# Kernel tuning notes

Measured on AMD Instinct MI355X. Metric: run time of the kernel, lower is better.

The kernel has to match this reference:

```python
import jax, jax.numpy as jnp
import numpy as np

N = 100000   # nodes
E = 1600000  # edges
F_IN = 128
H = 128
C_OUT = 10
G = 128      # graphs in batch
EPS = 1e-5


def setup_inputs() -> dict:
    key = jax.random.key(0)
    ks = jax.random.split(key, 16)
    x = jax.random.normal(ks[0], (N, F_IN), dtype=jnp.float32)
    edge_index = jax.random.randint(ks[1], (2, E), 0, N, dtype=jnp.int64)
    batch = jnp.sort(jax.random.randint(ks[2], (N,), 0, G, dtype=jnp.int64))
    s = 1.0 / np.sqrt(H)
    inp = {"x": x, "edge_index": edge_index, "batch": batch}
    # GCNConv weights/biases
    inp["w1"] = jax.random.normal(ks[3], (F_IN, H), jnp.float32) * s
    inp["b1"] = jax.random.normal(ks[4], (H,), jnp.float32) * 0.01
    inp["w2"] = jax.random.normal(ks[5], (H, H), jnp.float32) * s
    inp["b2"] = jax.random.normal(ks[6], (H,), jnp.float32) * 0.01
    inp["w3"] = jax.random.normal(ks[7], (H, H), jnp.float32) * s
    inp["b3"] = jax.random.normal(ks[8], (H,), jnp.float32) * 0.01
    # GraphNorm params: scale (weight), shift (bias), mean_scale (alpha)
    for i, k in zip((1, 2, 3), (ks[9], ks[10], ks[11])):
        kk = jax.random.split(k, 3)
        inp[f"g{i}w"] = 1.0 + 0.1 * jax.random.normal(kk[0], (H,), jnp.float32)
        inp[f"g{i}b"] = 0.1 * jax.random.normal(kk[1], (H,), jnp.float32)
        inp[f"g{i}a"] = 1.0 + 0.1 * jax.random.normal(kk[2], (H,), jnp.float32)
    inp["lw"] = jax.random.normal(ks[12], (H, C_OUT), jnp.float32) * s
    inp["lb"] = jax.random.normal(ks[13], (C_OUT,), jnp.float32) * 0.01
    return inp


def _gcn_norm(edge_index, n):
    # add self loops, symmetric normalization D^-1/2 (A+I) D^-1/2
    loop = jnp.arange(n, dtype=edge_index.dtype)
    src = jnp.concatenate([edge_index[0], loop])
    dst = jnp.concatenate([edge_index[1], loop])
    deg = jax.ops.segment_sum(jnp.ones_like(dst, dtype=jnp.float32), dst, num_segments=n)
    dinv = jnp.where(deg > 0, jax.lax.rsqrt(deg), 0.0)
    norm = dinv[src] * dinv[dst]
    return src, dst, norm


def _gcn_conv(x, w, b, src, dst, norm, n):
    h = x @ w                              # [N,H]
    msg = h[src] * norm[:, None]           # gather + edge weight
    out = jax.ops.segment_sum(msg, dst, num_segments=n)  # scatter-add
    return out + b


def _graph_norm(x, weight, bias, alpha, batch, cnt, g):
    mean = jax.ops.segment_sum(x, batch, num_segments=g) / cnt[:, None]
    sub = x - alpha * mean[batch]
    var = jax.ops.segment_sum(sub * sub, batch, num_segments=g) / cnt[:, None]
    return weight * sub * jax.lax.rsqrt(var[batch] + EPS) + bias


def reference(x, edge_index, batch, w1, b1, w2, b2, w3, b3,
              g1w, g1b, g1a, g2w, g2b, g2a, g3w, g3b, g3a, lw, lb):
    n = x.shape[0]
    src, dst, norm = _gcn_norm(edge_index, n)
    cnt = jnp.maximum(jax.ops.segment_sum(jnp.ones((n,), jnp.float32), batch, num_segments=G), 1.0)
    # dropout is identity in eval mode
    h = _gcn_conv(x, w1, b1, src, dst, norm, n)
    h = jax.nn.relu(_graph_norm(h, g1w, g1b, g1a, batch, cnt, G))
    h = _gcn_conv(h, w2, b2, src, dst, norm, n)
    h = jax.nn.relu(_graph_norm(h, g2w, g2b, g2a, batch, cnt, G))
    h = _gcn_conv(h, w3, b3, src, dst, norm, n)
    h = jax.nn.relu(_graph_norm(h, g3w, g3b, g3a, batch, cnt, G))
    pooled = jax.ops.segment_sum(h, batch, num_segments=G) / cnt[:, None]  # global_mean_pool
    logits = pooled @ lw + lb
    return jax.nn.log_softmax(logits, axis=1)
```

## Files before the change

### kernel.cpp

```cpp
#include <hip/hip_runtime.h>

#define NN 100000
#define NE 1600000
#define HD 128
#define NG 128
#define NC 10
#define EPSV 1e-5f

#define BSH 9
#define NBKT ((NN + 511) >> 9)
#define BIN_BLOCKS ((NE + 4095) / 4096)

typedef __attribute__((ext_vector_type(8))) short short8;
typedef __attribute__((ext_vector_type(4))) float f32x4;

__device__ __forceinline__ float b2f(ushort u){ return __uint_as_float(((unsigned)u)<<16); }
__device__ __forceinline__ ushort f2b(float f){
  unsigned u = __float_as_uint(f);
  unsigned r = (u + 0x7FFFu + ((u>>16)&1u)) >> 16;
  return (ushort)r;
}

__global__ __launch_bounds__(256)
void k_init(const int* __restrict__ batch, int* __restrict__ gstart,
            const float* __restrict__ w1, const float* __restrict__ w2,
            const float* __restrict__ w3, ushort* __restrict__ wT,
            int* __restrict__ gbhist, float* __restrict__ zero_base)
{
  int b = blockIdx.x, t = threadIdx.x;
  if(b < 391){
    int n = b*256 + t;
    if(n >= NN) return;
    int bb = batch[n];
    if(n == 0){
      for(int g=0; g<=bb; g++) gstart[g] = 0;
      int last = batch[NN-1];
      for(int g=last+1; g<=NG; g++) gstart[g] = NN;
    } else {
      int bp = batch[n-1];
      for(int g=bp+1; g<=bb; g++) gstart[g] = n;
    }
  } else if(b < 394){
    const float* w = (b == 391) ? w1 : (b == 392) ? w2 : w3;
    ushort* o = wT + (b-391)*16384;
    #pragma unroll 4
    for(int i=0;i<64;i++){
      int e = i*256 + t;
      int k = e>>7, h = e&127;
      o[h*128 + k] = f2b(w[e]);
    }
  } else if(b < 408){
    #pragma unroll 8
    for(int i=0;i<32;i++) zero_base[(size_t)(b-394)*8192 + i*256 + t] = 0.f;
  } else {
    if(t < NBKT) gbhist[t] = 0;
  }
}

__global__ __launch_bounds__(256) void k_bhist(const int* __restrict__ ei, int* __restrict__ gbhist){
  __shared__ int h[NBKT];
  int t = threadIdx.x;
  if(t < NBKT) h[t] = 0;
  __syncthreads();
  int base = blockIdx.x*4096;
  #pragma unroll
  for(int i=0;i<16;i++){
    int e = base + i*256 + t;
    if(e < NE) atomicAdd(&h[ei[NE + e] >> BSH], 1);
  }
  __syncthreads();
  if(t < NBKT && h[t]) atomicAdd(&gbhist[t], h[t]);
}

__global__ void k_bscan(const int* __restrict__ gbhist, int* __restrict__ bucket_base,
                        int* __restrict__ bucket_cursor, int* __restrict__ rowstart){
  __shared__ int lds[256];
  int t = threadIdx.x;
  int v = (t < NBKT) ? gbhist[t] : 0;
  lds[t] = v; __syncthreads();
  for(int off=1; off<256; off<<=1){
    int y = lds[t]; int z = (t>=off)?lds[t-off]:0;
    __syncthreads(); lds[t] = y+z; __syncthreads();
  }
  int excl = (t>0)?lds[t-1]:0;
  if(t < NBKT){ bucket_base[t] = excl; bucket_cursor[t] = excl; }
  if(t == 0){ bucket_base[NBKT] = NE; rowstart[NN] = NE; }
}

__global__ __launch_bounds__(256) void k_bin(const int* __restrict__ ei, int* __restrict__ bucket_cursor,
                                             unsigned* __restrict__ ebuf){
  __shared__ unsigned eb[4096];
  __shared__ unsigned char bb4[4096];
  __shared__ int hist[NBKT], lstart[NBKT], lcur[NBKT], rbase[NBKT];
  __shared__ int scanbuf[256];
  int t = threadIdx.x;
  if(t < NBKT) hist[t] = 0;
  __syncthreads();
  int base = blockIdx.x*4096;
  int nv = NE - base; if(nv > 4096) nv = 4096;
  int se[16], de[16];
  #pragma unroll
  for(int i=0;i<16;i++){
    int e = base + i*256 + t;
    if(e < NE){ se[i] = ei[e]; de[i] = ei[NE + e]; atomicAdd(&hist[de[i] >> BSH], 1); }
  }
  __syncthreads();
  int v = (t < NBKT) ? hist[t] : 0;
  scanbuf[t] = v; __syncthreads();
  for(int off=1; off<256; off<<=1){
    int y = scanbuf[t]; int z = (t>=off)?scanbuf[t-off]:0;
    __syncthreads(); scanbuf[t] = y+z; __syncthreads();
  }
  if(t < NBKT){
    int excl = (t>0)?scanbuf[t-1]:0;
    lstart[t] = excl; lcur[t] = excl;
    if(hist[t]) rbase[t] = atomicAdd(&bucket_cursor[t], hist[t]);
  }
  __syncthreads();
  #pragma unroll
  for(int i=0;i<16;i++){
    int e = base + i*256 + t;
    if(e < NE){
      int b = de[i] >> BSH;
      int idx = atomicAdd(&lcur[b], 1);
      eb[idx] = ((unsigned)(de[i] & 511) << 17) | (unsigned)se[i];
      bb4[idx] = (unsigned char)b;
    }
  }
  __syncthreads();
  #pragma unroll
  for(int i=0;i<16;i++){
    int slot = i*256 + t;
    if(slot < nv){
      int b = bb4[slot];
      ebuf[rbase[b] + (slot - lstart[b])] = eb[slot];
    }
  }
}

__global__ __launch_bounds__(256) void k_sort(const unsigned* __restrict__ ebuf,
                                              const int* __restrict__ bucket_base,
                                              int* __restrict__ srcs, int* __restrict__ rowstart,
                                              float* __restrict__ dinv){
  __shared__ int hist[512], cur[512];
  __shared__ int scanbuf[256];
  int b = blockIdx.x, t = threadIdx.x;
  int e0 = bucket_base[b], e1 = bucket_base[b+1];
  hist[t] = 0; hist[t+256] = 0;
  __syncthreads();
  for(int i = e0 + t; i < e1; i += 256){
    atomicAdd(&hist[ebuf[i] >> 17], 1);
  }
  __syncthreads();
  int s0 = hist[2*t], s1 = hist[2*t+1];
  scanbuf[t] = s0 + s1; __syncthreads();
  for(int off=1; off<256; off<<=1){
    int y = scanbuf[t]; int z = (t>=off)?scanbuf[t-off]:0;
    __syncthreads(); scanbuf[t] = y+z; __syncthreads();
  }
  int excl = (t>0)?scanbuf[t-1]:0;
  cur[2*t] = excl; cur[2*t+1] = excl + s0;
  int d0 = (b << BSH) + 2*t, d1 = d0 + 1;
  if(d0 < NN){ rowstart[d0] = e0 + excl;      dinv[d0] = rsqrtf((float)(s0 + 1)); }
  if(d1 < NN){ rowstart[d1] = e0 + excl + s0; dinv[d1] = rsqrtf((float)(s1 + 1)); }
  __syncthreads();
  for(int i = e0 + t; i < e1; i += 256){
    unsigned pk = ebuf[i];
    int dl = pk >> 17;
    int pos = e0 + atomicAdd(&cur[dl], 1);
    srcs[pos] = (int)(pk & 0x1FFFFu);
  }
}

template<int NORM>
__global__ __launch_bounds__(256)
void k_gemm(const void* __restrict__ in_, const ushort* __restrict__ wT,
            ushort* __restrict__ g, const float* __restrict__ dinv,
            const int* __restrict__ batch,
            const float* __restrict__ gw, const float* __restrict__ gb,
            const float* __restrict__ ga, const float* __restrict__ S1,
            const float* __restrict__ S2, const int* __restrict__ gstart)
{
  __shared__ ushort lds_a[128*136];
  __shared__ float sdinv[128];
  const int t = threadIdx.x;
  const int row0 = blockIdx.x * 128;

  {
    const int l = t & 31;
    const int rr = t >> 5;
    if(t < 128){
      int node = row0 + t;
      sdinv[t] = (node < NN) ? dinv[node] : 0.f;
    }
    float4 gwv, gbv, gav;
    float4 amv = make_float4(0.f,0.f,0.f,0.f), rsv = make_float4(0.f,0.f,0.f,0.f);
    int gprev = -1;
    if(NORM){
      gwv = ((const float4*)gw)[l]; gbv = ((const float4*)gb)[l];
      gav = ((const float4*)ga)[l];
    }
    #pragma unroll 4
    for(int rb = 0; rb < 16; rb++){
      int r = rb*8 + rr;
      int node = row0 + r;
      float4 v = make_float4(0.f,0.f,0.f,0.f);
      if(node < NN){
        if(NORM){
          ushort4 raw = ((const ushort4*)in_)[(size_t)node*32 + l];
          v = make_float4(b2f(raw.x), b2f(raw.y), b2f(raw.z), b2f(raw.w));
          int gg = batch[node];
          if(gg != gprev){
            gprev = gg;
            int c0 = gstart[gg], c1 = gstart[gg+1];
            float inv = 1.f/(float)((c1-c0) > 0 ? (c1-c0) : 1);
            float4 s1v = ((const float4*)S1)[gg*32 + l];
            float4 s2v = ((const float4*)S2)[gg*32 + l];
            float m, ex2, a;
            m = s1v.x*inv; ex2 = s2v.x*inv; a = gav.x;
            amv.x = a*m; rsv.x = rsqrtf(ex2 - (2.f*a - a*a)*m*m + EPSV);
            m = s1v.y*inv; ex2 = s2v.y*inv; a = gav.y;
            amv.y = a*m; rsv.y = rsqrtf(ex2 - (2.f*a - a*a)*m*m + EPSV);
            m = s1v.z*inv; ex2 = s2v.z*inv; a = gav.z;
            amv.z = a*m; rsv.z = rsqrtf(ex2 - (2.f*a - a*a)*m*m + EPSV);
            m = s1v.w*inv; ex2 = s2v.w*inv; a = gav.w;
            amv.w = a*m; rsv.w = rsqrtf(ex2 - (2.f*a - a*a)*m*m + EPSV);
          }
          v.x = fmaxf(gwv.x*(v.x-amv.x)*rsv.x + gbv.x, 0.f);
          v.y = fmaxf(gwv.y*(v.y-amv.y)*rsv.y + gbv.y, 0.f);
          v.z = fmaxf(gwv.z*(v.z-amv.z)*rsv.z + gbv.z, 0.f);
          v.w = fmaxf(gwv.w*(v.w-amv.w)*rsv.w + gbv.w, 0.f);
        } else {
          v = ((const float4*)in_)[(size_t)node*32 + l];
        }
      }
      ushort4 b4;
      b4.x = f2b(v.x); b4.y = f2b(v.y); b4.z = f2b(v.z); b4.w = f2b(v.w);
      *(ushort4*)(lds_a + r*136 + l*4) = b4;
    }
  }
  __syncthreads();

  const int wv = t >> 6;
  const int l  = t & 63;
  const int lc = l & 15, lk = l >> 4;

  short8 bfrag[2][4];
  #pragma unroll
  for(int tt=0; tt<2; tt++){
    int col = wv*32 + tt*16 + lc;
    #pragma unroll
    for(int s=0; s<4; s++)
      bfrag[tt][s] = *(const short8*)(wT + col*128 + s*32 + lk*8);
  }

  f32x4 acc[8][2];
  #pragma unroll
  for(int m=0;m<8;m++){ acc[m][0] = (f32x4)0.f; acc[m][1] = (f32x4)0.f; }

  #pragma unroll
  for(int m=0; m<8; m++){
    const ushort* ap = lds_a + (m*16 + lc)*136 + lk*8;
    #pragma unroll
    for(int s=0; s<4; s++){
      short8 a = *(const short8*)(ap + s*32);
      acc[m][0] = __builtin_amdgcn_mfma_f32_16x16x32_bf16(a, bfrag[0][s], acc[m][0], 0, 0, 0);
      acc[m][1] = __builtin_amdgcn_mfma_f32_16x16x32_bf16(a, bfrag[1][s], acc[m][1], 0, 0, 0);
    }
  }

  #pragma unroll
  for(int m=0; m<8; m++){
    #pragma unroll
    for(int tt=0; tt<2; tt++){
      int colg = wv*32 + tt*16 + lc;
      #pragma unroll
      for(int r=0; r<4; r++){
        int row = m*16 + lk*4 + r;
        int node = row0 + row;
        if(node < NN)
          g[(size_t)node*128 + colg] = f2b(acc[m][tt][r] * sdinv[row]);
      }
    }
  }
}

__global__ __launch_bounds__(256)
void k_agg(const ushort* __restrict__ g, const int* __restrict__ rowstart,
           const int* __restrict__ srcs, const float* __restrict__ dinv,
           const float* __restrict__ bias, ushort* __restrict__ outp)
{
  const int lane = threadIdx.x & 31;
  const int node = blockIdx.x*8 + (threadIdx.x >> 5);
  const int e0 = rowstart[node], e1 = rowstart[node+1];
  float ax=0.f, ay=0.f, az=0.f, aw=0.f;
  float bx=0.f, by=0.f, bz=0.f, bw=0.f;
  const ushort4* gp = (const ushort4*)g;
  int e = e0;
  for(; e+7 < e1; e += 8){
    int si[8];
    #pragma unroll
    for(int i=0;i<8;i++) si[i] = srcs[e+i];
    ushort4 v[8];
    #pragma unroll
    for(int i=0;i<8;i++) v[i] = gp[(size_t)si[i]*32 + lane];
    #pragma unroll
    for(int i=0;i<8;i++){
      if(i&1){ bx += b2f(v[i].x); by += b2f(v[i].y); bz += b2f(v[i].z); bw += b2f(v[i].w); }
      else   { ax += b2f(v[i].x); ay += b2f(v[i].y); az += b2f(v[i].z); aw += b2f(v[i].w); }
    }
  }
  for(; e+3 < e1; e += 4){
    int si[4];
    #pragma unroll
    for(int i=0;i<4;i++) si[i] = srcs[e+i];
    ushort4 v[4];
    #pragma unroll
    for(int i=0;i<4;i++) v[i] = gp[(size_t)si[i]*32 + lane];
    #pragma unroll
    for(int i=0;i<4;i++){
      if(i&1){ bx += b2f(v[i].x); by += b2f(v[i].y); bz += b2f(v[i].z); bw += b2f(v[i].w); }
      else   { ax += b2f(v[i].x); ay += b2f(v[i].y); az += b2f(v[i].z); aw += b2f(v[i].w); }
    }
  }
  for(; e < e1; e++){
    ushort4 v = gp[(size_t)srcs[e]*32 + lane];
    ax += b2f(v.x); ay += b2f(v.y); az += b2f(v.z); aw += b2f(v.w);
  }
  ushort4 vs = gp[(size_t)node*32 + lane];
  float dv = dinv[node];
  float4 bv = ((const float4*)bias)[lane];
  ushort4 o4;
  o4.x = f2b(dv*(ax+bx+b2f(vs.x))+bv.x);
  o4.y = f2b(dv*(ay+by+b2f(vs.y))+bv.y);
  o4.z = f2b(dv*(az+bz+b2f(vs.z))+bv.z);
  o4.w = f2b(dv*(aw+bw+b2f(vs.w))+bv.w);
  ((ushort4*)outp)[(size_t)node*32 + lane] = o4;
}

#define STAT_CH 8
__global__ __launch_bounds__(128)
void k_stats(const ushort* __restrict__ x, const int* __restrict__ gstart,
             float* __restrict__ S1, float* __restrict__ S2)
{
  int g = blockIdx.x, ch = blockIdx.y, f = threadIdx.x;
  int s = gstart[g], e = gstart[g+1];
  int len = e - s;
  int i0 = s + (int)((long long)len * ch / STAT_CH);
  int i1 = s + (int)((long long)len * (ch+1) / STAT_CH);
  float a1 = 0.f, a2 = 0.f;
  for(int n=i0; n<i1; n++){
    float v = b2f(x[(size_t)n*128 + f]);
    a1 += v; a2 += v*v;
  }
  if(i1 > i0){
    atomicAdd(&S1[g*128+f], a1);
    atomicAdd(&S2[g*128+f], a2);
  }
}

#define POOL_CH 16
__global__ __launch_bounds__(128)
void k_pool(const ushort* __restrict__ x, const int* __restrict__ gstart,
            const float* __restrict__ gw, const float* __restrict__ gb,
            const float* __restrict__ ga, const float* __restrict__ S1,
            const float* __restrict__ S2, float* __restrict__ pooled)
{
  int g = blockIdx.x, ch = blockIdx.y, f = threadIdx.x;
  int s = gstart[g], e = gstart[g+1];
  int len = e - s;
  int i0 = s + (int)((long long)len * ch / POOL_CH);
  int i1 = s + (int)((long long)len * (ch+1) / POOL_CH);
  float inv = 1.f/(float)(len > 0 ? len : 1);
  float a = ga[f];
  float m = S1[g*128+f]*inv, ex2 = S2[g*128+f]*inv;
  float am = a*m;
  float rs = rsqrtf(ex2 - (2.f*a - a*a)*m*m + EPSV);
  float wv = gw[f], bv = gb[f];
  float a1 = 0.f;
  for(int n=i0; n<i1; n++){
    float v = b2f(x[(size_t)n*128 + f]);
    v = wv*(v-am)*rs + bv;
    a1 += fmaxf(v, 0.f);
  }
  if(i1 > i0) atomicAdd(&pooled[g*128+f], a1);
}

__global__ __launch_bounds__(64)
void k_head(const float* __restrict__ pooled, const int* __restrict__ gstart,
            const float* __restrict__ lw, const float* __restrict__ lb,
            float* __restrict__ out)
{
  int g = blockIdx.x, t = threadIdx.x;
  __shared__ float lg[NC];
  __shared__ float lse_s;
  int len = gstart[g+1] - gstart[g];
  float inv = 1.f/(float)(len > 0 ? len : 1);
  if(t < NC){
    float acc = lb[t];
    for(int f=0; f<128; f++) acc += pooled[g*128+f]*inv*lw[f*NC + t];
    lg[t] = acc;
  }
  __syncthreads();
  if(t == 0){
    float mx = -1e30f;
    for(int c=0;c<NC;c++) mx = fmaxf(mx, lg[c]);
    float sm = 0.f;
    for(int c=0;c<NC;c++) sm += expf(lg[c]-mx);
    lse_s = mx + logf(sm);
  }
  __syncthreads();
  if(t < NC) out[g*NC + t] = lg[t] - lse_s;
}

extern "C" void kernel_launch(void* const* d_in, const int* in_sizes, int n_in,
                              void* d_out, int out_size, void* d_ws, size_t ws_size,
                              hipStream_t stream)
{
  const float* x    = (const float*)d_in[0];
  const int*   ei   = (const int*)d_in[1];
  const int*   batch= (const int*)d_in[2];
  const float* w1   = (const float*)d_in[3];
  const float* b1   = (const float*)d_in[4];
  const float* w2   = (const float*)d_in[5];
  const float* b2   = (const float*)d_in[6];
  const float* w3   = (const float*)d_in[7];
  const float* b3   = (const float*)d_in[8];
  const float* g1w  = (const float*)d_in[9];
  const float* g1b  = (const float*)d_in[10];
  const float* g1a  = (const float*)d_in[11];
  const float* g2w  = (const float*)d_in[12];
  const float* g2b  = (const float*)d_in[13];
  const float* g2a  = (const float*)d_in[14];
  const float* g3w  = (const float*)d_in[15];
  const float* g3b  = (const float*)d_in[16];
  const float* g3a  = (const float*)d_in[17];
  const float* lw   = (const float*)d_in[18];
  const float* lb   = (const float*)d_in[19];
  float* out = (float*)d_out;

  char* p = (char*)d_ws;
  auto take = [&](size_t nbytes){ char* q = p; p += (nbytes + 255) & ~(size_t)255; return q; };
  ushort* gbuf    = (ushort*)take((size_t)NN*HD*2);
  ushort* bufB    = (ushort*)take((size_t)NN*HD*2);
  ushort* wT      = (ushort*)take((size_t)3*HD*HD*2);
  unsigned* ebuf  = (unsigned*)take((size_t)NE*4);
  int*   srcs     = (int*)  take((size_t)NE*4);
  int*   rowstart = (int*)  take((size_t)(NN+1)*4);
  float* dinv     = (float*)take((size_t)NN*4);
  int*   gbhist   = (int*)  take((size_t)NBKT*4);
  int*   bucket_base   = (int*)take((size_t)(NBKT+1)*4);
  int*   bucket_cursor = (int*)take((size_t)NBKT*4);
  int*   gstart   = (int*)  take((size_t)(NG+1)*4);
  float* Sbase    = (float*)take((size_t)(3*2*NG*HD + NG*HD)*4);
  if((size_t)(p - (char*)d_ws) > ws_size) return;

  float* SL1 = Sbase;
  float* SL2 = Sbase + 2*NG*HD;
  float* SL3 = Sbase + 4*NG*HD;
  float* pooled = Sbase + 6*NG*HD;

  k_init  <<<409, 256, 0, stream>>>(batch, gstart, w1, w2, w3, wT, gbhist, Sbase);
  k_bhist <<<BIN_BLOCKS, 256, 0, stream>>>(ei, gbhist);
  k_bscan <<<1, 256, 0, stream>>>(gbhist, bucket_base, bucket_cursor, rowstart);
  k_bin   <<<BIN_BLOCKS, 256, 0, stream>>>(ei, bucket_cursor, ebuf);
  k_sort  <<<NBKT, 256, 0, stream>>>(ebuf, bucket_base, srcs, rowstart, dinv);

  const int GB = (NN + 127)/128;
  const int AB = NN/8;

  k_gemm<0><<<GB, 256, 0, stream>>>(x, wT, gbuf, dinv, batch,
                                    nullptr, nullptr, nullptr, nullptr, nullptr, gstart);
  k_agg<<<AB, 256, 0, stream>>>(gbuf, rowstart, srcs, dinv, b1, bufB);
  k_stats<<<dim3(NG, STAT_CH), 128, 0, stream>>>(bufB, gstart, SL1, SL1 + NG*HD);

  k_gemm<1><<<GB, 256, 0, stream>>>(bufB, wT + 16384, gbuf, dinv, batch,
                                    g1w, g1b, g1a, SL1, SL1 + NG*HD, gstart);
  k_agg<<<AB, 256, 0, stream>>>(gbuf, rowstart, srcs, dinv, b2, bufB);
  k_stats<<<dim3(NG, STAT_CH), 128, 0, stream>>>(bufB, gstart, SL2, SL2 + NG*HD);

  k_gemm<1><<<GB, 256, 0, stream>>>(bufB, wT + 32768, gbuf, dinv, batch,
                                    g2w, g2b, g2a, SL2, SL2 + NG*HD, gstart);
  k_agg<<<AB, 256, 0, stream>>>(gbuf, rowstart, srcs, dinv, b3, bufB);
  k_stats<<<dim3(NG, STAT_CH), 128, 0, stream>>>(bufB, gstart, SL3, SL3 + NG*HD);

  k_pool<<<dim3(NG, POOL_CH), 128, 0, stream>>>(bufB, gstart, g3w, g3b, g3a,
                                                SL3, SL3 + NG*HD, pooled);
  k_head<<<NG, 64, 0, stream>>>(pooled, gstart, lw, lb, out);
}
```

Measured before the change: 436.5 us.

## Fuse preprocessing and per-layer stages into persistent cooperative kernels with grid syncs

Replaces the five preprocessing launches with one cooperative kernel that uses grid.sync between init, histogram, scan, bin and sort phases. It also merges each layer's gemm, aggregation and stats launches, plus pool and head on the last layer, into one persistent cooperative kernel that loops over tiles. The gemm tile shrinks to 64 rows, and B fragments are loaded once per block. The aim is to remove per-kernel launch gaps and tail effects, at the cost of grid-wide barrier overhead and lower parallelism in the small phases. If a cooperative launch fails, the code falls back to the original separate kernels.

```diff
diff --git a/kernel.cpp b/kernel.cpp
--- a/kernel.cpp
+++ b/kernel.cpp
@@ -1,4 +1,7 @@
 #include <hip/hip_runtime.h>
+#include <hip/hip_cooperative_groups.h>
+
+namespace cg = cooperative_groups;
 
 #define NN 100000
 #define NE 1600000
@@ -10,6 +13,8 @@
 #define BSH 9
 #define NBKT ((NN + 511) >> 9)
 #define BIN_BLOCKS ((NE + 4095) / 4096)
+#define STAT_CH 8
+#define POOL_CH 16
 
 typedef __attribute__((ext_vector_type(8))) short short8;
 typedef __attribute__((ext_vector_type(4))) float f32x4;
@@ -20,6 +25,40 @@
   unsigned r = (u + 0x7FFFu + ((u>>16)&1u)) >> 16;
   return (ushort)r;
 }
+
+
+__device__ __forceinline__ void init_body(int vb, int t, const int* batch, int* gstart,
+    const float* w1, const float* w2, const float* w3, ushort* wT, int* gbhist, float* zero_base)
+{
+  if(vb < 391){
+    int n = vb*256 + t;
+    if(n < NN){
+      int bb = batch[n];
+      if(n == 0){
+        for(int g=0; g<=bb; g++) gstart[g] = 0;
+        int last = batch[NN-1];
+        for(int g=last+1; g<=NG; g++) gstart[g] = NN;
+      } else {
+        int bp = batch[n-1];
+        for(int g=bp+1; g<=bb; g++) gstart[g] = n;
+      }
+    }
+  } else if(vb < 394){
+    const float* w = (vb == 391) ? w1 : (vb == 392) ? w2 : w3;
+    ushort* o = wT + (vb-391)*16384;
+    #pragma unroll 4
+    for(int i=0;i<64;i++){
+      int e = i*256 + t;
+      o[(e & 127)*128 + (e >> 7)] = f2b(w[e]);
+    }
+  } else if(vb < 408){
+    #pragma unroll 8
+    for(int i=0;i<32;i++) zero_base[(size_t)(vb-394)*8192 + i*256 + t] = 0.f;
+  } else {
+    if(t < NBKT) gbhist[t] = 0;
+  }
+}
+
 
 __global__ __launch_bounds__(256)
 void k_init(const int* __restrict__ batch, int* __restrict__ gstart,
@@ -27,34 +66,7 @@
             const float* __restrict__ w3, ushort* __restrict__ wT,
             int* __restrict__ gbhist, float* __restrict__ zero_base)
 {
-  int b = blockIdx.x, t = threadIdx.x;
-  if(b < 391){
-    int n = b*256 + t;
-    if(n >= NN) return;
-    int bb = batch[n];
-    if(n == 0){
-      for(int g=0; g<=bb; g++) gstart[g] = 0;
-      int last = batch[NN-1];
-      for(int g=last+1; g<=NG; g++) gstart[g] = NN;
-    } else {
-      int bp = batch[n-1];
-      for(int g=bp+1; g<=bb; g++) gstart[g] = n;
-    }
-  } else if(b < 394){
-    const float* w = (b == 391) ? w1 : (b == 392) ? w2 : w3;
-    ushort* o = wT + (b-391)*16384;
-    #pragma unroll 4
-    for(int i=0;i<64;i++){
-      int e = i*256 + t;
-      int k = e>>7, h = e&127;
-      o[h*128 + k] = f2b(w[e]);
-    }
-  } else if(b < 408){
-    #pragma unroll 8
-    for(int i=0;i<32;i++) zero_base[(size_t)(b-394)*8192 + i*256 + t] = 0.f;
-  } else {
-    if(t < NBKT) gbhist[t] = 0;
-  }
+  init_body(blockIdx.x, threadIdx.x, batch, gstart, w1, w2, w3, wT, gbhist, zero_base);
 }
 
 __global__ __launch_bounds__(256) void k_bhist(const int* __restrict__ ei, int* __restrict__ gbhist){
@@ -148,9 +160,8 @@
   int e0 = bucket_base[b], e1 = bucket_base[b+1];
   hist[t] = 0; hist[t+256] = 0;
   __syncthreads();
-  for(int i = e0 + t; i < e1; i += 256){
+  for(int i = e0 + t; i < e1; i += 256)
     atomicAdd(&hist[ebuf[i] >> 17], 1);
-  }
   __syncthreads();
   int s0 = hist[2*t], s1 = hist[2*t+1];
   scanbuf[t] = s0 + s1; __syncthreads();
@@ -185,7 +196,6 @@
   __shared__ float sdinv[128];
   const int t = threadIdx.x;
   const int row0 = blockIdx.x * 128;
-
   {
     const int l = t & 31;
     const int rr = t >> 5;
@@ -241,10 +251,7 @@
   }
   __syncthreads();
 
-  const int wv = t >> 6;
-  const int l  = t & 63;
-  const int lc = l & 15, lk = l >> 4;
-
+  const int wv = t >> 6, l = t & 63, lc = l & 15, lk = l >> 4;
   short8 bfrag[2][4];
   #pragma unroll
   for(int tt=0; tt<2; tt++){
@@ -253,11 +260,9 @@
     for(int s=0; s<4; s++)
       bfrag[tt][s] = *(const short8*)(wT + col*128 + s*32 + lk*8);
   }
-
   f32x4 acc[8][2];
   #pragma unroll
   for(int m=0;m<8;m++){ acc[m][0] = (f32x4)0.f; acc[m][1] = (f32x4)0.f; }
-
   #pragma unroll
   for(int m=0; m<8; m++){
     const ushort* ap = lds_a + (m*16 + lc)*136 + lk*8;
@@ -268,7 +273,6 @@
       acc[m][1] = __builtin_amdgcn_mfma_f32_16x16x32_bf16(a, bfrag[1][s], acc[m][1], 0, 0, 0);
     }
   }
-
   #pragma unroll
   for(int m=0; m<8; m++){
     #pragma unroll
@@ -338,7 +342,6 @@
   ((ushort4*)outp)[(size_t)node*32 + lane] = o4;
 }
 
-#define STAT_CH 8
 __global__ __launch_bounds__(128)
 void k_stats(const ushort* __restrict__ x, const int* __restrict__ gstart,
              float* __restrict__ S1, float* __restrict__ S2)
@@ -359,7 +362,6 @@
   }
 }
 
-#define POOL_CH 16
 __global__ __launch_bounds__(128)
 void k_pool(const ushort* __restrict__ x, const int* __restrict__ gstart,
             const float* __restrict__ gw, const float* __restrict__ gb,
@@ -411,6 +413,372 @@
   }
   __syncthreads();
   if(t < NC) out[g*NC + t] = lg[t] - lse_s;
+}
+
+
+__global__ __launch_bounds__(256)
+void k_prep(const int* __restrict__ ei, const int* __restrict__ batch, int* __restrict__ gstart,
+            const float* __restrict__ w1, const float* __restrict__ w2, const float* __restrict__ w3,
+            ushort* __restrict__ wT, int* __restrict__ gbhist, float* __restrict__ zero_base,
+            int* __restrict__ bucket_base, int* __restrict__ bucket_cursor, int* __restrict__ rowstart,
+            unsigned* __restrict__ ebuf, int* __restrict__ srcs, float* __restrict__ dinv)
+{
+  __shared__ unsigned eb[4096];
+  __shared__ unsigned char bb4[4096];
+  __shared__ int hist[512];
+  __shared__ int cur[512];
+  __shared__ int lstart[NBKT];
+  __shared__ int rbase[NBKT];
+  __shared__ int scanbuf[256];
+  cg::grid_group grid = cg::this_grid();
+  const int t = threadIdx.x;
+
+  for(int vb = blockIdx.x; vb < 409; vb += gridDim.x)
+    init_body(vb, t, batch, gstart, w1, w2, w3, wT, gbhist, zero_base);
+  grid.sync();
+
+  for(int vb = blockIdx.x; vb < BIN_BLOCKS; vb += gridDim.x){
+    if(t < NBKT) hist[t] = 0;
+    __syncthreads();
+    int base = vb*4096;
+    #pragma unroll
+    for(int i=0;i<16;i++){
+      int e = base + i*256 + t;
+      if(e < NE) atomicAdd(&hist[ei[NE + e] >> BSH], 1);
+    }
+    __syncthreads();
+    if(t < NBKT && hist[t]) atomicAdd(&gbhist[t], hist[t]);
+    __syncthreads();
+  }
+  grid.sync();
+
+  if(blockIdx.x == 0){
+    int v = (t < NBKT) ? gbhist[t] : 0;
+    scanbuf[t] = v; __syncthreads();
+    for(int off=1; off<256; off<<=1){
+      int y = scanbuf[t]; int z = (t>=off)?scanbuf[t-off]:0;
+      __syncthreads(); scanbuf[t] = y+z; __syncthreads();
+    }
+    int excl = (t>0)?scanbuf[t-1]:0;
+    if(t < NBKT){ bucket_base[t] = excl; bucket_cursor[t] = excl; }
+    if(t == 0){ bucket_base[NBKT] = NE; rowstart[NN] = NE; }
+  }
+  grid.sync();
+
+  for(int vb = blockIdx.x; vb < BIN_BLOCKS; vb += gridDim.x){
+    if(t < NBKT) hist[t] = 0;
+    __syncthreads();
+    int base = vb*4096;
+    int nv = NE - base; if(nv > 4096) nv = 4096;
+    int se[16], de[16];
+    #pragma unroll
+    for(int i=0;i<16;i++){
+      int e = base + i*256 + t;
+      if(e < NE){ se[i] = ei[e]; de[i] = ei[NE + e]; atomicAdd(&hist[de[i] >> BSH], 1); }
+    }
+    __syncthreads();
+    int v = (t < NBKT) ? hist[t] : 0;
+    scanbuf[t] = v; __syncthreads();
+    for(int off=1; off<256; off<<=1){
+      int y = scanbuf[t]; int z = (t>=off)?scanbuf[t-off]:0;
+      __syncthreads(); scanbuf[t] = y+z; __syncthreads();
+    }
+    if(t < NBKT){
+      int excl = (t>0)?scanbuf[t-1]:0;
+      lstart[t] = excl; cur[t] = excl;
+      if(hist[t]) rbase[t] = atomicAdd(&bucket_cursor[t], hist[t]);
+    }
+    __syncthreads();
+    #pragma unroll
+    for(int i=0;i<16;i++){
+      int e = base + i*256 + t;
+      if(e < NE){
+        int b = de[i] >> BSH;
+        int idx = atomicAdd(&cur[b], 1);
+        eb[idx] = ((unsigned)(de[i] & 511) << 17) | (unsigned)se[i];
+        bb4[idx] = (unsigned char)b;
+      }
+    }
+    __syncthreads();
+    #pragma unroll
+    for(int i=0;i<16;i++){
+      int slot = i*256 + t;
+      if(slot < nv){
+        int b = bb4[slot];
+        ebuf[rbase[b] + (slot - lstart[b])] = eb[slot];
+      }
+    }
+    __syncthreads();
+  }
+  grid.sync();
+
+  for(int vb = blockIdx.x; vb < NBKT; vb += gridDim.x){
+    int e0 = bucket_base[vb], e1 = bucket_base[vb+1];
+    hist[t] = 0; hist[t+256] = 0;
+    __syncthreads();
+    for(int i = e0 + t; i < e1; i += 256)
+      atomicAdd(&hist[ebuf[i] >> 17], 1);
+    __syncthreads();
+    int s0 = hist[2*t], s1 = hist[2*t+1];
+    scanbuf[t] = s0 + s1; __syncthreads();
+    for(int off=1; off<256; off<<=1){
+      int y = scanbuf[t]; int z = (t>=off)?scanbuf[t-off]:0;
+      __syncthreads(); scanbuf[t] = y+z; __syncthreads();
+    }
+    int excl = (t>0)?scanbuf[t-1]:0;
+    cur[2*t] = excl; cur[2*t+1] = excl + s0;
+    int d0 = (vb << BSH) + 2*t, d1 = d0 + 1;
+    if(d0 < NN){ rowstart[d0] = e0 + excl;      dinv[d0] = rsqrtf((float)(s0 + 1)); }
+    if(d1 < NN){ rowstart[d1] = e0 + excl + s0; dinv[d1] = rsqrtf((float)(s1 + 1)); }
+    __syncthreads();
+    for(int i = e0 + t; i < e1; i += 256){
+      unsigned pk = ebuf[i];
+      int dl = pk >> 17;
+      int pos = e0 + atomicAdd(&cur[dl], 1);
+      srcs[pos] = (int)(pk & 0x1FFFFu);
+    }
+    __syncthreads();
+  }
+}
+
+template<int NORM, int LAST>
+__global__ __launch_bounds__(256, 4)
+void k_layer(const void* in_, const ushort* __restrict__ wTl,
+             ushort* gbuf, ushort* outB,
+             const float* __restrict__ dinv, const int* __restrict__ batch,
+             const int* __restrict__ gstart, const int* __restrict__ rowstart,
+             const int* __restrict__ srcs, const float* __restrict__ bias,
+             const float* __restrict__ gw, const float* __restrict__ gb,
+             const float* __restrict__ ga, const float* S1p, const float* S2p,
+             float* S1c, float* S2c,
+             const float* __restrict__ pw, const float* __restrict__ pb,
+             const float* __restrict__ pa, float* __restrict__ pooled,
+             const float* __restrict__ lw, const float* __restrict__ lb,
+             float* __restrict__ out)
+{
+  __shared__ ushort lds_a[64*136];
+  __shared__ float sdinv[64];
+  __shared__ float shead[NC+1];
+  cg::grid_group grid = cg::this_grid();
+  const int t = threadIdx.x;
+  const int wv = t >> 6, l = t & 63, lc = l & 15, lk = l >> 4;
+
+  short8 bfrag[2][4];
+  #pragma unroll
+  for(int tt=0; tt<2; tt++){
+    int col = wv*32 + tt*16 + lc;
+    #pragma unroll
+    for(int s=0; s<4; s++)
+      bfrag[tt][s] = *(const short8*)(wTl + col*128 + s*32 + lk*8);
+  }
+
+  for(int tile = blockIdx.x; tile < (NN+63)/64; tile += gridDim.x){
+    const int row0 = tile * 64;
+    {
+      const int sl = t & 31;
+      const int rr = t >> 5;
+      if(t < 64){
+        int node = row0 + t;
+        sdinv[t] = (node < NN) ? dinv[node] : 0.f;
+      }
+      float4 gwv, gbv, gav;
+      float4 amv = make_float4(0.f,0.f,0.f,0.f), rsv = make_float4(0.f,0.f,0.f,0.f);
+      int gprev = -1;
+      if(NORM){
+        gwv = ((const float4*)gw)[sl]; gbv = ((const float4*)gb)[sl];
+        gav = ((const float4*)ga)[sl];
+      }
+      #pragma unroll 4
+      for(int rb = 0; rb < 8; rb++){
+        int r = rb*8 + rr;
+        int node = row0 + r;
+        float4 v = make_float4(0.f,0.f,0.f,0.f);
+        if(node < NN){
+          if(NORM){
+            ushort4 raw = ((const ushort4*)in_)[(size_t)node*32 + sl];
+            v = make_float4(b2f(raw.x), b2f(raw.y), b2f(raw.z), b2f(raw.w));
+            int gg = batch[node];
+            if(gg != gprev){
+              gprev = gg;
+              int c0 = gstart[gg], c1 = gstart[gg+1];
+              float inv = 1.f/(float)((c1-c0) > 0 ? (c1-c0) : 1);
+              float4 s1v = ((const float4*)S1p)[gg*32 + sl];
+              float4 s2v = ((const float4*)S2p)[gg*32 + sl];
+              float m, ex2, a;
+              m = s1v.x*inv; ex2 = s2v.x*inv; a = gav.x;
+              amv.x = a*m; rsv.x = rsqrtf(ex2 - (2.f*a - a*a)*m*m + EPSV);
+              m = s1v.y*inv; ex2 = s2v.y*inv; a = gav.y;
+              amv.y = a*m; rsv.y = rsqrtf(ex2 - (2.f*a - a*a)*m*m + EPSV);
+              m = s1v.z*inv; ex2 = s2v.z*inv; a = gav.z;
+              amv.z = a*m; rsv.z = rsqrtf(ex2 - (2.f*a - a*a)*m*m + EPSV);
+              m = s1v.w*inv; ex2 = s2v.w*inv; a = gav.w;
+              amv.w = a*m; rsv.w = rsqrtf(ex2 - (2.f*a - a*a)*m*m + EPSV);
+            }
+            v.x = fmaxf(gwv.x*(v.x-amv.x)*rsv.x + gbv.x, 0.f);
+            v.y = fmaxf(gwv.y*(v.y-amv.y)*rsv.y + gbv.y, 0.f);
+            v.z = fmaxf(gwv.z*(v.z-amv.z)*rsv.z + gbv.z, 0.f);
+            v.w = fmaxf(gwv.w*(v.w-amv.w)*rsv.w + gbv.w, 0.f);
+          } else {
+            v = ((const float4*)in_)[(size_t)node*32 + sl];
+          }
+        }
+        ushort4 b4;
+        b4.x = f2b(v.x); b4.y = f2b(v.y); b4.z = f2b(v.z); b4.w = f2b(v.w);
+        *(ushort4*)(lds_a + r*136 + sl*4) = b4;
+      }
+    }
+    __syncthreads();
+
+    f32x4 acc[4][2];
+    #pragma unroll
+    for(int m=0;m<4;m++){ acc[m][0] = (f32x4)0.f; acc[m][1] = (f32x4)0.f; }
+    #pragma unroll
+    for(int m=0; m<4; m++){
+      const ushort* ap = lds_a + (m*16 + lc)*136 + lk*8;
+      #pragma unroll
+      for(int s=0; s<4; s++){
+        short8 a = *(const short8*)(ap + s*32);
+        acc[m][0] = __builtin_amdgcn_mfma_f32_16x16x32_bf16(a, bfrag[0][s], acc[m][0], 0, 0, 0);
+        acc[m][1] = __builtin_amdgcn_mfma_f32_16x16x32_bf16(a, bfrag[1][s], acc[m][1], 0, 0, 0);
+      }
+    }
+    #pragma unroll
+    for(int m=0; m<4; m++){
+      #pragma unroll
+      for(int tt=0; tt<2; tt++){
+        int colg = wv*32 + tt*16 + lc;
+        #pragma unroll
+        for(int r=0; r<4; r++){
+          int row = m*16 + lk*4 + r;
+          int node = row0 + row;
+          if(node < NN)
+            gbuf[(size_t)node*128 + colg] = f2b(acc[m][tt][r] * sdinv[row]);
+        }
+      }
+    }
+    __syncthreads();
+  }
+  grid.sync();
+
+  {
+    const int lane = t & 31;
+    const ushort4* gp = (const ushort4*)gbuf;
+    for(int grp = blockIdx.x; grp < NN/8; grp += gridDim.x){
+      const int node = grp*8 + (t >> 5);
+      const int e0 = rowstart[node], e1 = rowstart[node+1];
+      float ax=0.f, ay=0.f, az=0.f, aw=0.f;
+      float bx=0.f, by=0.f, bz=0.f, bw=0.f;
+      int e = e0;
+      for(; e+7 < e1; e += 8){
+        int si[8];
+        #pragma unroll
+        for(int i=0;i<8;i++) si[i] = srcs[e+i];
+        ushort4 v[8];
+        #pragma unroll
+        for(int i=0;i<8;i++) v[i] = gp[(size_t)si[i]*32 + lane];
+        #pragma unroll
+        for(int i=0;i<8;i++){
+          if(i&1){ bx += b2f(v[i].x); by += b2f(v[i].y); bz += b2f(v[i].z); bw += b2f(v[i].w); }
+          else   { ax += b2f(v[i].x); ay += b2f(v[i].y); az += b2f(v[i].z); aw += b2f(v[i].w); }
+        }
+      }
+      for(; e+3 < e1; e += 4){
+        int si[4];
+        #pragma unroll
+        for(int i=0;i<4;i++) si[i] = srcs[e+i];
+        ushort4 v[4];
+        #pragma unroll
+        for(int i=0;i<4;i++) v[i] = gp[(size_t)si[i]*32 + lane];
+        #pragma unroll
+        for(int i=0;i<4;i++){
+          if(i&1){ bx += b2f(v[i].x); by += b2f(v[i].y); bz += b2f(v[i].z); bw += b2f(v[i].w); }
+          else   { ax += b2f(v[i].x); ay += b2f(v[i].y); az += b2f(v[i].z); aw += b2f(v[i].w); }
+        }
+      }
+      for(; e < e1; e++){
+        ushort4 v = gp[(size_t)srcs[e]*32 + lane];
+        ax += b2f(v.x); ay += b2f(v.y); az += b2f(v.z); aw += b2f(v.w);
+      }
+      ushort4 vs = gp[(size_t)node*32 + lane];
+      float dv = dinv[node];
+      float4 bv = ((const float4*)bias)[lane];
+      ushort4 o4;
+      o4.x = f2b(dv*(ax+bx+b2f(vs.x))+bv.x);
+      o4.y = f2b(dv*(ay+by+b2f(vs.y))+bv.y);
+      o4.z = f2b(dv*(az+bz+b2f(vs.z))+bv.z);
+      o4.w = f2b(dv*(aw+bw+b2f(vs.w))+bv.w);
+      ((ushort4*)outB)[(size_t)node*32 + lane] = o4;
+    }
+  }
+  grid.sync();
+
+  {
+    const int f = t & 127, sub = t >> 7;
+    for(int idx = blockIdx.x; idx < NG*STAT_CH; idx += gridDim.x){
+      int g = idx >> 3, ch = idx & 7;
+      int s = gstart[g], e = gstart[g+1];
+      int len = e - s;
+      int i0 = s + (int)((long long)len * ch / STAT_CH);
+      int i1 = s + (int)((long long)len * (ch+1) / STAT_CH);
+      float a1 = 0.f, a2 = 0.f;
+      for(int n = i0 + sub; n < i1; n += 2){
+        float v = b2f(outB[(size_t)n*128 + f]);
+        a1 += v; a2 += v*v;
+      }
+      if(i1 > i0){
+        atomicAdd(&S1c[g*128+f], a1);
+        atomicAdd(&S2c[g*128+f], a2);
+      }
+    }
+  }
+
+  if(LAST){
+    grid.sync();
+    {
+      const int f = t & 127, sub = t >> 7;
+      for(int idx = blockIdx.x; idx < NG*POOL_CH; idx += gridDim.x){
+        int g = idx >> 4, ch = idx & 15;
+        int s = gstart[g], e = gstart[g+1];
+        int len = e - s;
+        int i0 = s + (int)((long long)len * ch / POOL_CH);
+        int i1 = s + (int)((long long)len * (ch+1) / POOL_CH);
+        float inv = 1.f/(float)(len > 0 ? len : 1);
+        float a = pa[f];
+        float m = S1c[g*128+f]*inv, ex2 = S2c[g*128+f]*inv;
+        float am = a*m;
+        float rs = rsqrtf(ex2 - (2.f*a - a*a)*m*m + EPSV);
+        float wvv = pw[f], bvv = pb[f];
+        float a1 = 0.f;
+        for(int n = i0 + sub; n < i1; n += 2){
+          float v = b2f(outB[(size_t)n*128 + f]);
+          v = wvv*(v-am)*rs + bvv;
+          a1 += fmaxf(v, 0.f);
+        }
+        if(i1 > i0) atomicAdd(&pooled[g*128+f], a1);
+      }
+    }
+    grid.sync();
+    for(int g = blockIdx.x; g < NG; g += gridDim.x){
+      int len = gstart[g+1] - gstart[g];
+      float inv = 1.f/(float)(len > 0 ? len : 1);
+      if(t < NC){
+        float acc = lb[t];
+        for(int f2=0; f2<128; f2++) acc += pooled[g*128+f2]*inv*lw[f2*NC + t];
+        shead[t] = acc;
+      }
+      __syncthreads();
+      if(t == 0){
+        float mx = -1e30f;
+        for(int c=0;c<NC;c++) mx = fmaxf(mx, shead[c]);
+        float sm = 0.f;
+        for(int c=0;c<NC;c++) sm += expf(shead[c]-mx);
+        shead[NC] = mx + logf(sm);
+      }
+      __syncthreads();
+      if(t < NC) out[g*NC + t] = shead[t] - shead[NC];
+      __syncthreads();
+    }
+  }
 }
 
 extern "C" void kernel_launch(void* const* d_in, const int* in_sizes, int n_in,
@@ -455,36 +823,96 @@
   float* Sbase    = (float*)take((size_t)(3*2*NG*HD + NG*HD)*4);
   if((size_t)(p - (char*)d_ws) > ws_size) return;
 
-  float* SL1 = Sbase;
-  float* SL2 = Sbase + 2*NG*HD;
-  float* SL3 = Sbase + 4*NG*HD;
+  float* SL1  = Sbase;
+  float* SL1b = Sbase + 1*NG*HD;
+  float* SL2  = Sbase + 2*NG*HD;
+  float* SL2b = Sbase + 3*NG*HD;
+  float* SL3  = Sbase + 4*NG*HD;
+  float* SL3b = Sbase + 5*NG*HD;
   float* pooled = Sbase + 6*NG*HD;
 
-  k_init  <<<409, 256, 0, stream>>>(batch, gstart, w1, w2, w3, wT, gbhist, Sbase);
-  k_bhist <<<BIN_BLOCKS, 256, 0, stream>>>(ei, gbhist);
-  k_bscan <<<1, 256, 0, stream>>>(gbhist, bucket_base, bucket_cursor, rowstart);
-  k_bin   <<<BIN_BLOCKS, 256, 0, stream>>>(ei, bucket_cursor, ebuf);
-  k_sort  <<<NBKT, 256, 0, stream>>>(ebuf, bucket_base, srcs, rowstart, dinv);
+  int nbP = 0, nbL0 = 0, nbL1 = 0, nbL2 = 0;
+  (void)hipOccupancyMaxActiveBlocksPerMultiprocessor(&nbP,  k_prep,        256, 0);
+  (void)hipOccupancyMaxActiveBlocksPerMultiprocessor(&nbL0, k_layer<0,0>,  256, 0);
+  (void)hipOccupancyMaxActiveBlocksPerMultiprocessor(&nbL1, k_layer<1,0>,  256, 0);
+  (void)hipOccupancyMaxActiveBlocksPerMultiprocessor(&nbL2, k_layer<1,1>,  256, 0);
+  int nbL = nbL0 < nbL1 ? nbL0 : nbL1; if(nbL2 < nbL) nbL = nbL2;
+  const int NCU = 256;
+  long long capL = (long long)nbL * NCU;
+  int GL = (int)(capL < 2048 ? capL : 2048);
+
+  bool prep_ok = false;
+  if(nbP > 0 && (long long)nbP * NCU >= 409){
+    void* args[] = {(void*)&ei, (void*)&batch, (void*)&gstart, (void*)&w1, (void*)&w2,
+                    (void*)&w3, (void*)&wT, (void*)&gbhist, (void*)&Sbase,
+                    (void*)&bucket_base, (void*)&bucket_cursor, (void*)&rowstart,
+                    (void*)&ebuf, (void*)&srcs, (void*)&dinv};
+    prep_ok = (hipLaunchCooperativeKernel(k_prep, dim3(409), dim3(256), args, 0, stream) == hipSuccess);
+  }
+  if(!prep_ok){
+    k_init  <<<409, 256, 0, stream>>>(batch, gstart, w1, w2, w3, wT, gbhist, Sbase);
+    k_bhist <<<BIN_BLOCKS, 256, 0, stream>>>(ei, gbhist);
+    k_bscan <<<1, 256, 0, stream>>>(gbhist, bucket_base, bucket_cursor, rowstart);
+    k_bin   <<<BIN_BLOCKS, 256, 0, stream>>>(ei, bucket_cursor, ebuf);
+    k_sort  <<<NBKT, 256, 0, stream>>>(ebuf, bucket_base, srcs, rowstart, dinv);
+  }
 
   const int GB = (NN + 127)/128;
   const int AB = NN/8;
 
-  k_gemm<0><<<GB, 256, 0, stream>>>(x, wT, gbuf, dinv, batch,
-                                    nullptr, nullptr, nullptr, nullptr, nullptr, gstart);
-  k_agg<<<AB, 256, 0, stream>>>(gbuf, rowstart, srcs, dinv, b1, bufB);
-  k_stats<<<dim3(NG, STAT_CH), 128, 0, stream>>>(bufB, gstart, SL1, SL1 + NG*HD);
-
-  k_gemm<1><<<GB, 256, 0, stream>>>(bufB, wT + 16384, gbuf, dinv, batch,
-                                    g1w, g1b, g1a, SL1, SL1 + NG*HD, gstart);
-  k_agg<<<AB, 256, 0, stream>>>(gbuf, rowstart, srcs, dinv, b2, bufB);
-  k_stats<<<dim3(NG, STAT_CH), 128, 0, stream>>>(bufB, gstart, SL2, SL2 + NG*HD);
-
-  k_gemm<1><<<GB, 256, 0, stream>>>(bufB, wT + 32768, gbuf, dinv, batch,
-                                    g2w, g2b, g2a, SL2, SL2 + NG*HD, gstart);
-  k_agg<<<AB, 256, 0, stream>>>(gbuf, rowstart, srcs, dinv, b3, bufB);
-  k_stats<<<dim3(NG, STAT_CH), 128, 0, stream>>>(bufB, gstart, SL3, SL3 + NG*HD);
-
-  k_pool<<<dim3(NG, POOL_CH), 128, 0, stream>>>(bufB, gstart, g3w, g3b, g3a,
-                                                SL3, SL3 + NG*HD, pooled);
-  k_head<<<NG, 64, 0, stream>>>(pooled, gstart, lw, lb, out);
-}
+  bool ok = false;
+  if(GL > 0){
+    const void* inp = (const void*)x;
+    const ushort* wTl = wT;
+    void* args[] = {(void*)&inp, (void*)&wTl, (void*)&gbuf, (void*)&bufB, (void*)&dinv,
+                    (void*)&batch, (void*)&gstart, (void*)&rowstart, (void*)&srcs, (void*)&b1,
+                    (void*)&g1w, (void*)&g1b, (void*)&g1a, (void*)&SL1, (void*)&SL1b,
+                    (void*)&SL1, (void*)&SL1b, (void*)&g3w, (void*)&g3b, (void*)&g3a,
+                    (void*)&pooled, (void*)&lw, (void*)&lb, (void*)&out};
+    ok = (hipLaunchCooperativeKernel(k_layer<0,0>, dim3(GL), dim3(256), args, 0, stream) == hipSuccess);
+  }
+  if(!ok){
+    k_gemm<0><<<GB, 256, 0, stream>>>(x, wT, gbuf, dinv, batch,
+                                      nullptr, nullptr, nullptr, nullptr, nullptr, gstart);
+    k_agg<<<AB, 256, 0, stream>>>(gbuf, rowstart, srcs, dinv, b1, bufB);
+    k_stats<<<dim3(NG, STAT_CH), 128, 0, stream>>>(bufB, gstart, SL1, SL1b);
+  }
+
+  ok = false;
+  if(GL > 0){
+    const void* inp = (const void*)bufB;
+    const ushort* wTl = wT + 16384;
+    void* args[] = {(void*)&inp, (void*)&wTl, (void*)&gbuf, (void*)&bufB, (void*)&dinv,
+                    (void*)&batch, (void*)&gstart, (void*)&rowstart, (void*)&srcs, (void*)&b2,
+                    (void*)&g1w, (void*)&g1b, (void*)&g1a, (void*)&SL1, (void*)&SL1b,
+                    (void*)&SL2, (void*)&SL2b, (void*)&g3w, (void*)&g3b, (void*)&g3a,
+                    (void*)&pooled, (void*)&lw, (void*)&lb, (void*)&out};
+    ok = (hipLaunchCooperativeKernel(k_layer<1,0>, dim3(GL), dim3(256), args, 0, stream) == hipSuccess);
+  }
+  if(!ok){
+    k_gemm<1><<<GB, 256, 0, stream>>>(bufB, wT + 16384, gbuf, dinv, batch,
+                                      g1w, g1b, g1a, SL1, SL1b, gstart);
+    k_agg<<<AB, 256, 0, stream>>>(gbuf, rowstart, srcs, dinv, b2, bufB);
+    k_stats<<<dim3(NG, STAT_CH), 128, 0, stream>>>(bufB, gstart, SL2, SL2b);
+  }
+
+  ok = false;
+  if(GL > 0){
+    const void* inp = (const void*)bufB;
+    const ushort* wTl = wT + 32768;
+    void* args[] = {(void*)&inp, (void*)&wTl, (void*)&gbuf, (void*)&bufB, (void*)&dinv,
+                    (void*)&batch, (void*)&gstart, (void*)&rowstart, (void*)&srcs, (void*)&b3,
+                    (void*)&g2w, (void*)&g2b, (void*)&g2a, (void*)&SL2, (void*)&SL2b,
+                    (void*)&SL3, (void*)&SL3b, (void*)&g3w, (void*)&g3b, (void*)&g3a,
+                    (void*)&pooled, (void*)&lw, (void*)&lb, (void*)&out};
+    ok = (hipLaunchCooperativeKernel(k_layer<1,1>, dim3(GL), dim3(256), args, 0, stream) == hipSuccess);
+  }
+  if(!ok){
+    k_gemm<1><<<GB, 256, 0, stream>>>(bufB, wT + 32768, gbuf, dinv, batch,
+                                      g2w, g2b, g2a, SL2, SL2b, gstart);
+    k_agg<<<AB, 256, 0, stream>>>(gbuf, rowstart, srcs, dinv, b3, bufB);
+    k_stats<<<dim3(NG, STAT_CH), 128, 0, stream>>>(bufB, gstart, SL3, SL3b);
+    k_pool<<<dim3(NG, POOL_CH), 128, 0, stream>>>(bufB, gstart, g3w, g3b, g3a, SL3, SL3b, pooled);
+    k_head<<<NG, 64, 0, stream>>>(pooled, gstart, lw, lb, out);
+  }
+}
```

After: 1.284 ms. 194% more time.
